# Kernel tuning notes

Hardware: AMD Instinct MI355X
Metric: run time of the kernel (lower is better)

Reference implementation:

```python
import jax, jax.numpy as jnp
import numpy as np

B, N, M, K = 4, 8192, 2048, 8
F1, F2 = 256, 256


def _knn_idx(p1t, p2t, k):
    # p1t [B,N,3], p2t [B,M,3] -> idx [B,N,k] of k nearest points in p2t for each p1t point
    d = (jnp.sum(p1t ** 2, -1)[:, :, None]
         + jnp.sum(p2t ** 2, -1)[:, None, :]
         - 2.0 * jnp.einsum('bnc,bmc->bnm', p1t, p2t))
    _, idx = jax.lax.top_k(-d, k)
    return idx


def _gather(feat, idx):
    # feat [B,C,M], idx [B,N,K] -> [B,C,N,K]  (grouping_operation)
    return jax.vmap(lambda f, i: f[:, i])(feat, idx)


def setup_inputs() -> dict:
    key = jax.random.key(0)
    ks = jax.random.split(key, 16)
    rn = lambda k, s: jax.random.normal(k, s, dtype=jnp.float32)
    ru = lambda k, s: jax.random.uniform(k, s, dtype=jnp.float32)
    return {
        'pos1': rn(ks[0], (B, 3, N)),
        'pos2': rn(ks[1], (B, 3, M)),
        'feature1': rn(ks[2], (B, F1, N)),
        'feature2': rn(ks[3], (B, F2, M)),
        'w1_0': rn(ks[4], (128, F2 + 3)) * 0.05, 's1_0': ru(ks[5], (128,)), 'b1_0': rn(ks[6], (128,)) * 0.05,
        'w1_1': rn(ks[7], (128, 128)) * 0.05, 's1_1': ru(ks[8], (128,)), 'b1_1': rn(ks[9], (128,)) * 0.05,
        'w1_2': rn(ks[10], (256, 128)) * 0.05, 's1_2': ru(ks[11], (256,)), 'b1_2': rn(ks[12], (256,)) * 0.05,
        'w2_0': rn(ks[13], (256, 256 + F1)) * 0.05, 's2_0': ru(ks[14], (256,)), 'b2_0': rn(ks[15], (256,)) * 0.05,
    }


def reference(pos1, pos2, feature1, feature2,
              w1_0, s1_0, b1_0, w1_1, s1_1, b1_1, w1_2, s1_2, b1_2,
              w2_0, s2_0, b2_0):
    # KNN grouping (knn=True branch): neighbors of each pos1 point among pos2 points
    idx = _knn_idx(pos1.transpose(0, 2, 1), pos2.transpose(0, 2, 1), K)  # [B,N,K]
    pos2_grouped = _gather(pos2, idx)                 # [B,3,N,K]
    pos_diff = pos2_grouped - pos1[:, :, :, None]     # [B,3,N,K]
    feat2_grouped = _gather(feature2, idx)            # [B,F2,N,K]
    feat = jnp.concatenate([feat2_grouped, pos_diff], axis=1)  # [B,F2+3,N,K]
    # mlp1: 1x1 Conv2d (no bias) + BN(eval, folded scale/bias) + ReLU
    for w, s, b in ((w1_0, s1_0, b1_0), (w1_1, s1_1, b1_1), (w1_2, s1_2, b1_2)):
        feat = jax.nn.relu(jnp.einsum('oc,bcnk->bonk', w, feat)
                           * s[None, :, None, None] + b[None, :, None, None])
    feat = jnp.max(feat, axis=-1)                     # [B,256,N]
    feat = jnp.concatenate([feat, feature1], axis=1)  # [B,256+F1,N]
    # mlp2: 1x1 Conv1d (no bias) + BN + ReLU
    for w, s, b in ((w2_0, s2_0, b2_0),):
        feat = jax.nn.relu(jnp.einsum('oc,bcn->bon', w, feat)
                           * s[None, :, None] + b[None, :, None])
    return feat
```

## Files before the change

### kernel.cpp

```cpp
#include <hip/hip_runtime.h>
#include <hip/hip_bf16.h>

#define B_ 4
#define N_ 8192
#define M_ 2048
#define K_ 8

typedef __bf16 bf16x8 __attribute__((ext_vector_type(8)));
typedef __bf16 bf16x4 __attribute__((ext_vector_type(4)));
typedef float  floatx4 __attribute__((ext_vector_type(4)));
typedef unsigned long long u64k;

__global__ __launch_bounds__(256) void preproc(
    const float* __restrict__ w10, const float* __restrict__ w11,
    const float* __restrict__ w12, const float* __restrict__ w20,
    const float* __restrict__ feature2,
    __bf16* __restrict__ w0p, __bf16* __restrict__ w11b,
    __bf16* __restrict__ w12b, __bf16* __restrict__ w20b,
    __bf16* __restrict__ f2t)
{
  __shared__ float tile[32][33];
  const int bid = blockIdx.x;
  if (bid < 2048) {
    const int C = 256, L = M_;
    const int b = bid >> 9;
    const int c0 = ((bid >> 6) & 7) * 32, l0 = (bid & 63) * 32;
    const int tx = threadIdx.x & 31, ty = threadIdx.x >> 5;
    const float* src = feature2 + (size_t)b * C * L;
    #pragma unroll
    for (int i = 0; i < 4; i++)
      tile[ty + 8 * i][tx] = src[(size_t)(c0 + ty + 8 * i) * L + l0 + tx];
    __syncthreads();
    __bf16* dst = f2t + (size_t)b * L * C;
    #pragma unroll
    for (int i = 0; i < 4; i++)
      dst[(size_t)(l0 + ty + 8 * i) * C + c0 + tx] = (__bf16)tile[tx][ty + 8 * i];
  } else {
    int t = (bid - 2048) * 256 + threadIdx.x;
    if (t < 36864) {
      int o = t / 288, c = t - o * 288;
      w0p[t] = (c < 259) ? (__bf16)w10[o * 259 + c] : (__bf16)0.0f;
    } else if (t < 53248) {
      int i = t - 36864; w11b[i] = (__bf16)w11[i];
    } else if (t < 86016) {
      int i = t - 53248; w12b[i] = (__bf16)w12[i];
    } else if (t < 217088) {
      int i = t - 86016; w20b[i] = (__bf16)w20[i];
    }
  }
}

__device__ __forceinline__ void ce(u64k& a, u64k& b) {
  u64k lo = a < b ? a : b;
  u64k hi = a < b ? b : a;
  a = lo; b = hi;
}

__global__ __launch_bounds__(256, 4) void knn_kernel(
    const float* __restrict__ pos1, const float* __restrict__ pos2,
    u64k* __restrict__ part)
{
  __shared__ floatx4 P[1024];
  __shared__ u64k md[64][33];
  const int b = blockIdx.y;
  const int half = blockIdx.z;
  const int n0 = blockIdx.x * 64;
  const int tid = threadIdx.x;
  const int cbase = half * 1024;

  const float* p2 = pos2 + b * 3 * M_;
  for (int i = tid; i < 1024; i += 256) {
    const int c = cbase + i;
    float x = p2[c], y = p2[M_ + c], z = p2[2 * M_ + c];
    floatx4 q;
    q[0] = x; q[1] = y; q[2] = z;
    q[3] = __fadd_rn(__fadd_rn(__fmul_rn(x, x), __fmul_rn(y, y)), __fmul_rn(z, z));
    P[i] = q;
  }
  __syncthreads();

  const int p = tid >> 2, t = tid & 3;
  const int n = n0 + p;
  const float* p1 = pos1 + b * 3 * N_;
  const float x1 = p1[n], y1 = p1[N_ + n], z1 = p1[2 * N_ + n];
  const float r1 = __fadd_rn(__fadd_rn(__fmul_rn(x1, x1), __fmul_rn(y1, y1)),
                             __fmul_rn(z1, z1));

  u64k bd[8];
  #pragma unroll
  for (int r = 0; r < 8; r++) bd[r] = ~0ULL;

  for (int bb = 0; bb < 32; ++bb) {
    floatx4 q[8];
    #pragma unroll
    for (int i = 0; i < 8; i++) q[i] = P[4 * (8 * bb + i) + t];

    u64k s[8];
    #pragma unroll
    for (int i = 0; i < 8; i++) {
      float dot = __fadd_rn(__fadd_rn(__fmul_rn(x1, q[i][0]), __fmul_rn(y1, q[i][1])),
                            __fmul_rn(z1, q[i][2]));
      float d = __fsub_rn(__fadd_rn(r1, q[i][3]), __fmul_rn(2.0f, dot));
      unsigned du = __float_as_uint(d);
      unsigned k32 = du ^ ((unsigned)((int)du >> 31) | 0x80000000u);
      s[i] = ((u64k)k32 << 11) | (unsigned)(cbase + 4 * (8 * bb + i) + t);
    }

    ce(s[0], s[1]); ce(s[2], s[3]); ce(s[4], s[5]); ce(s[6], s[7]);
    ce(s[0], s[2]); ce(s[1], s[3]); ce(s[4], s[6]); ce(s[5], s[7]);
    ce(s[1], s[2]); ce(s[5], s[6]);
    ce(s[0], s[4]); ce(s[1], s[5]); ce(s[2], s[6]); ce(s[3], s[7]);
    ce(s[2], s[4]); ce(s[3], s[5]);
    ce(s[1], s[2]); ce(s[3], s[4]); ce(s[5], s[6]);

    if (s[0] < bd[7]) {
      #pragma unroll
      for (int k = 0; k < 8; k++) { u64k x = s[7 - k]; bd[k] = bd[k] < x ? bd[k] : x; }
      ce(bd[0], bd[4]); ce(bd[1], bd[5]); ce(bd[2], bd[6]); ce(bd[3], bd[7]);
      ce(bd[0], bd[2]); ce(bd[1], bd[3]); ce(bd[4], bd[6]); ce(bd[5], bd[7]);
      ce(bd[0], bd[1]); ce(bd[2], bd[3]); ce(bd[4], bd[5]); ce(bd[6], bd[7]);
    }
  }

  #pragma unroll
  for (int r = 0; r < 8; r++) md[p][t * 8 + r] = bd[r];
  __syncthreads();

  if (tid < 64) {
    int h0 = 0, h1 = 0, h2 = 0, h3 = 0;
    u64k* o = part + ((size_t)((b * 2 + half) * N_ + n0 + tid)) * 8;
    #pragma unroll
    for (int r = 0; r < 8; r++) {
      u64k k0 = md[tid][h0], k1 = md[tid][8 + h1];
      u64k k2 = md[tid][16 + h2], k3 = md[tid][24 + h3];
      u64k m01 = k0 < k1 ? k0 : k1;
      u64k m23 = k2 < k3 ? k2 : k3;
      u64k m = m01 < m23 ? m01 : m23;
      h0 += (k0 == m); h1 += (k1 == m); h2 += (k2 == m); h3 += (k3 == m);
      o[r] = m;
    }
  }
}

template <int KSTEPS>
__device__ __forceinline__ void mfma_kloop_swz(
    const __bf16* X, const __bf16* W, int wstride, int c0, int lane,
    floatx4 (&acc)[4][2])
{
  const int lrow = lane & 15, quad = lane >> 4;
  const floatx4 fz = {0.f, 0.f, 0.f, 0.f};
  #pragma unroll
  for (int pt = 0; pt < 4; pt++) { acc[pt][0] = fz; acc[pt][1] = fz; }

  bf16x8 wf0 = *(const bf16x8*)(W + (size_t)(c0 + lrow) * wstride + quad * 8);
  bf16x8 wf1 = *(const bf16x8*)(W + (size_t)(c0 + 16 + lrow) * wstride + quad * 8);
  bf16x8 xf[4];
  #pragma unroll
  for (int pt = 0; pt < 4; pt++) {
    const int row = pt * 16 + lrow;
    xf[pt] = *(const bf16x8*)((const char*)X + row * 256
                              + ((quad * 16) ^ ((row & 7) << 4)));
  }

  #pragma unroll
  for (int ks = 0; ks < KSTEPS; ks++) {
    bf16x8 wn0, wn1, xn[4];
    if (ks + 1 < KSTEPS) {
      const int kn = (ks + 1) * 32 + quad * 8;
      wn0 = *(const bf16x8*)(W + (size_t)(c0 + lrow) * wstride + kn);
      wn1 = *(const bf16x8*)(W + (size_t)(c0 + 16 + lrow) * wstride + kn);
      #pragma unroll
      for (int pt = 0; pt < 4; pt++) {
        const int row = pt * 16 + lrow;
        xn[pt] = *(const bf16x8*)((const char*)X + row * 256
                                  + (((ks + 1) * 64 + quad * 16) ^ ((row & 7) << 4)));
      }
    }
    #pragma unroll
    for (int pt = 0; pt < 4; pt++) {
      acc[pt][0] = __builtin_amdgcn_mfma_f32_16x16x32_bf16(wf0, xf[pt], acc[pt][0], 0, 0, 0);
      acc[pt][1] = __builtin_amdgcn_mfma_f32_16x16x32_bf16(wf1, xf[pt], acc[pt][1], 0, 0, 0);
    }
    if (ks + 1 < KSTEPS) {
      wf0 = wn0; wf1 = wn1;
      #pragma unroll
      for (int pt = 0; pt < 4; pt++) xf[pt] = xn[pt];
    }
  }
}

__global__ __launch_bounds__(256, 3) void mlp1_kernel(
    const float* __restrict__ pos1, const float* __restrict__ pos2,
    const u64k* __restrict__ part, const __bf16* __restrict__ f2t,
    const __bf16* __restrict__ w0p, const float* __restrict__ s10, const float* __restrict__ b10,
    const __bf16* __restrict__ w11b, const float* __restrict__ s11, const float* __restrict__ b11,
    const __bf16* __restrict__ w12b, const float* __restrict__ s12, const float* __restrict__ b12,
    __bf16* __restrict__ maxed)
{
  __shared__ __align__(16) __bf16 Xs[64 * 256];
  __shared__ int mrow[64];
  __bf16* const Y1 = Xs;
  __bf16* const Y0 = Xs + 32 * 256;
  __bf16* const Mst = Xs + 32 * 256;

  const int b = blockIdx.y;
  const int n0 = blockIdx.x * 8;
  const int tid = threadIdx.x;
  const int wave = tid >> 6, lane = tid & 63;
  const int lrow = lane & 15, quad = lane >> 4;
  const int c0 = 32 * wave;

  if (tid < 8) {
    const u64k* a0 = part + ((size_t)((b * 2 + 0) * N_ + n0 + tid)) * 8;
    const u64k* a1 = part + ((size_t)((b * 2 + 1) * N_ + n0 + tid)) * 8;
    u64k av[8], cv[8];
    #pragma unroll
    for (int r = 0; r < 8; r++) { av[r] = a0[r]; cv[r] = a1[r]; }
    #pragma unroll
    for (int k = 0; k < 8; k++) { u64k x = cv[7 - k]; av[k] = av[k] < x ? av[k] : x; }
    ce(av[0], av[4]); ce(av[1], av[5]); ce(av[2], av[6]); ce(av[3], av[7]);
    ce(av[0], av[2]); ce(av[1], av[3]); ce(av[4], av[6]); ce(av[5], av[7]);
    ce(av[0], av[1]); ce(av[2], av[3]); ce(av[4], av[5]); ce(av[6], av[7]);
    #pragma unroll
    for (int r = 0; r < 8; r++) mrow[tid * 8 + r] = (int)(av[r] & 2047u);
  }
  __syncthreads();

  {
    const int r0 = wave * 16;
    const int hf = lane >> 5;
    const int ch = lane & 31;
    #pragma unroll
    for (int i = 0; i < 8; i++) {
      const int r = r0 + 2 * i + hf;
      const int m = mrow[r];
      const char* src = (const char*)f2t
          + (((size_t)(b * M_ + m)) << 9)
          + ((ch << 4) ^ ((r & 7) << 4));
      __builtin_amdgcn_global_load_lds(
          (const __attribute__((address_space(1))) unsigned int*)src,
          (__attribute__((address_space(3))) unsigned int*)(Xs + (r0 + 2 * i) * 256),
          16, 0, 0);
    }
  }

  bf16x8 xlast[4];
  #pragma unroll
  for (int pt = 0; pt < 4; pt++) { bf16x8 v = {}; xlast[pt] = v; }
  if (quad == 0) {
    #pragma unroll
    for (int pt = 0; pt < 4; pt++) {
      const int r = pt * 16 + lrow;
      const int m = mrow[r];
      const int n = n0 + (r >> 3);
      bf16x8 v = {};
      v[0] = (__bf16)(pos2[b * 3 * M_ + m]          - pos1[b * 3 * N_ + n]);
      v[1] = (__bf16)(pos2[b * 3 * M_ + M_ + m]     - pos1[b * 3 * N_ + N_ + n]);
      v[2] = (__bf16)(pos2[b * 3 * M_ + 2 * M_ + m] - pos1[b * 3 * N_ + 2 * N_ + n]);
      xlast[pt] = v;
    }
  }

  bf16x8 wf0 = *(const bf16x8*)(w0p + (size_t)(c0 + lrow) * 288 + quad * 8);
  bf16x8 wf1 = *(const bf16x8*)(w0p + (size_t)(c0 + 16 + lrow) * 288 + quad * 8);

  __syncthreads();

  floatx4 acc[4][2];
  {
    const floatx4 fz = {0.f, 0.f, 0.f, 0.f};
    #pragma unroll
    for (int pt = 0; pt < 4; pt++) { acc[pt][0] = fz; acc[pt][1] = fz; }

    const int swz = (lrow & 7) << 4;
    bf16x8 xf[4];
    #pragma unroll
    for (int pt = 0; pt < 4; pt++)
      xf[pt] = *(const bf16x8*)((const char*)Xs + (pt * 16 + lrow) * 512
                                + ((quad * 16) ^ swz));

    #pragma unroll
    for (int ks = 0; ks < 9; ks++) {
      bf16x8 wn0, wn1, xn[4];
      if (ks < 8) {
        const int kn = (ks + 1) * 32 + quad * 8;
        wn0 = *(const bf16x8*)(w0p + (size_t)(c0 + lrow) * 288 + kn);
        wn1 = *(const bf16x8*)(w0p + (size_t)(c0 + 16 + lrow) * 288 + kn);
        if (ks < 7) {
          const int kb = ((ks + 1) * 64 + quad * 16) ^ swz;
          #pragma unroll
          for (int pt = 0; pt < 4; pt++)
            xn[pt] = *(const bf16x8*)((const char*)Xs + (pt * 16 + lrow) * 512 + kb);
        } else {
          #pragma unroll
          for (int pt = 0; pt < 4; pt++) xn[pt] = xlast[pt];
        }
      }
      #pragma unroll
      for (int pt = 0; pt < 4; pt++) {
        acc[pt][0] = __builtin_amdgcn_mfma_f32_16x16x32_bf16(wf0, xf[pt], acc[pt][0], 0, 0, 0);
        acc[pt][1] = __builtin_amdgcn_mfma_f32_16x16x32_bf16(wf1, xf[pt], acc[pt][1], 0, 0, 0);
      }
      if (ks < 8) {
        wf0 = wn0; wf1 = wn1;
        #pragma unroll
        for (int pt = 0; pt < 4; pt++) xf[pt] = xn[pt];
      }
    }
  }

  __syncthreads();

  #pragma unroll
  for (int pt = 0; pt < 4; pt++) {
    #pragma unroll
    for (int wt = 0; wt < 2; wt++) {
      const int colg = c0 + wt * 16 + quad * 4;
      floatx4 s4 = *(const floatx4*)(s10 + colg);
      floatx4 b4 = *(const floatx4*)(b10 + colg);
      bf16x4 pk;
      #pragma unroll
      for (int r = 0; r < 4; r++) {
        float v = acc[pt][wt][r] * s4[r] + b4[r];
        pk[r] = (__bf16)(v > 0.f ? v : 0.f);
      }
      const int row = pt * 16 + lrow;
      const int cb = colg * 2;
      *(bf16x4*)((char*)Y0 + row * 256
                 + ((cb & ~15) ^ ((row & 7) << 4)) + (cb & 15)) = pk;
    }
  }
  __syncthreads();

  {
    floatx4 a1c[4][2];
    mfma_kloop_swz<4>(Y0, w11b, 128, c0, lane, a1c);
    #pragma unroll
    for (int pt = 0; pt < 4; pt++) {
      #pragma unroll
      for (int wt = 0; wt < 2; wt++) {
        const int colg = c0 + wt * 16 + quad * 4;
        floatx4 s4 = *(const floatx4*)(s11 + colg);
        floatx4 b4 = *(const floatx4*)(b11 + colg);
        bf16x4 pk;
        #pragma unroll
        for (int r = 0; r < 4; r++) {
          float v = a1c[pt][wt][r] * s4[r] + b4[r];
          pk[r] = (__bf16)(v > 0.f ? v : 0.f);
        }
        const int row = pt * 16 + lrow;
        const int cb = colg * 2;
        *(bf16x4*)((char*)Y1 + row * 256
                   + ((cb & ~15) ^ ((row & 7) << 4)) + (cb & 15)) = pk;
      }
    }
  }
  __syncthreads();

  #pragma unroll
  for (int p = 0; p < 2; p++) {
    floatx4 a2c[4][2];
    mfma_kloop_swz<4>(Y1, w12b, 128, 128 * p + c0, lane, a2c);
    #pragma unroll
    for (int pt = 0; pt < 4; pt++) {
      #pragma unroll
      for (int wt = 0; wt < 2; wt++) {
        const int colg = 128 * p + c0 + wt * 16 + quad * 4;
        floatx4 s4 = *(const floatx4*)(s12 + colg);
        floatx4 b4 = *(const floatx4*)(b12 + colg);
        floatx4 v;
        #pragma unroll
        for (int r = 0; r < 4; r++) {
          float t = a2c[pt][wt][r] * s4[r] + b4[r];
          v[r] = t > 0.f ? t : 0.f;
        }
        #pragma unroll
        for (int st = 1; st <= 4; st <<= 1) {
          #pragma unroll
          for (int r = 0; r < 4; r++)
            v[r] = fmaxf(v[r], __shfl_xor(v[r], st, 64));
        }
        if ((lrow & 7) == 0) {
          const int point = pt * 2 + (lrow >> 3);
          bf16x4 pk;
          #pragma unroll
          for (int r = 0; r < 4; r++) pk[r] = (__bf16)v[r];
          *(bf16x4*)(Mst + point * 264 + colg) = pk;
        }
      }
    }
  }
  __syncthreads();

  {
    const int point = tid >> 5, ch = tid & 31;
    bf16x8 v = *(const bf16x8*)(Mst + point * 264 + ch * 8);
    *(bf16x8*)(maxed + ((size_t)(b * N_ + n0 + point)) * 256 + ch * 8) = v;
  }
}

__global__ __launch_bounds__(256, 4) void mlp2_kernel(
    const __bf16* __restrict__ maxed, const float* __restrict__ feature1,
    const __bf16* __restrict__ w20b, const float* __restrict__ s20,
    const float* __restrict__ b20, float* __restrict__ out)
{
  const int rows0 = blockIdx.x * 32;
  const int b = rows0 >> 13;
  const int nbase = rows0 & (N_ - 1);
  const int tid = threadIdx.x;
  const int wave = tid >> 6, lane = tid & 63;
  const int lrow = lane & 15, quad = lane >> 4;
  const int c0 = 128 * blockIdx.y + 32 * wave;
  const floatx4 fz = {0.f, 0.f, 0.f, 0.f};

  floatx4 acc[2][2];
  acc[0][0] = fz; acc[0][1] = fz; acc[1][0] = fz; acc[1][1] = fz;

  auto afrag = [&](int ks, int mt) -> bf16x8 {
    const int k = ks * 32 + quad * 8;
    if (ks < 8) {
      return *(const bf16x8*)(maxed + (size_t)(rows0 + mt * 16 + lrow) * 256 + k);
    } else {
      const int c = k - 256;
      const float* p = feature1 + ((size_t)(b * 256 + c)) * N_
                       + (nbase + mt * 16 + lrow);
      bf16x8 v;
      #pragma unroll
      for (int j = 0; j < 8; j++) v[j] = (__bf16)p[(size_t)j * N_];
      return v;
    }
  };

  bf16x8 w0 = *(const bf16x8*)(w20b + (size_t)(c0 + lrow) * 512 + quad * 8);
  bf16x8 w1 = *(const bf16x8*)(w20b + (size_t)(c0 + 16 + lrow) * 512 + quad * 8);
  bf16x8 a0 = afrag(0, 0);
  bf16x8 a1 = afrag(0, 1);

  #pragma unroll
  for (int ks = 0; ks < 16; ks++) {
    bf16x8 wn0, wn1, an0, an1;
    if (ks < 15) {
      const int kn = (ks + 1) * 32 + quad * 8;
      wn0 = *(const bf16x8*)(w20b + (size_t)(c0 + lrow) * 512 + kn);
      wn1 = *(const bf16x8*)(w20b + (size_t)(c0 + 16 + lrow) * 512 + kn);
      an0 = afrag(ks + 1, 0);
      an1 = afrag(ks + 1, 1);
    }
    acc[0][0] = __builtin_amdgcn_mfma_f32_16x16x32_bf16(a0, w0, acc[0][0], 0, 0, 0);
    acc[0][1] = __builtin_amdgcn_mfma_f32_16x16x32_bf16(a0, w1, acc[0][1], 0, 0, 0);
    acc[1][0] = __builtin_amdgcn_mfma_f32_16x16x32_bf16(a1, w0, acc[1][0], 0, 0, 0);
    acc[1][1] = __builtin_amdgcn_mfma_f32_16x16x32_bf16(a1, w1, acc[1][1], 0, 0, 0);
    if (ks < 15) { w0 = wn0; w1 = wn1; a0 = an0; a1 = an1; }
  }

  #pragma unroll
  for (int ct = 0; ct < 2; ct++) {
    const int col = c0 + ct * 16 + lrow;
    const float s = s20[col];
    const float bb = b20[col];
    #pragma unroll
    for (int mt = 0; mt < 2; mt++) {
      floatx4 pk;
      #pragma unroll
      for (int r = 0; r < 4; r++) {
        float v = acc[mt][ct][r] * s + bb;
        pk[r] = v > 0.f ? v : 0.f;
      }
      const int n = nbase + mt * 16 + quad * 4;
      *(floatx4*)(out + ((size_t)(b * 256 + col)) * N_ + n) = pk;
    }
  }
}

extern "C" void kernel_launch(void* const* d_in, const int* in_sizes, int n_in,
                              void* d_out, int out_size, void* d_ws, size_t ws_size,
                              hipStream_t stream)
{
  const float* pos1     = (const float*)d_in[0];
  const float* pos2     = (const float*)d_in[1];
  const float* feature1 = (const float*)d_in[2];
  const float* feature2 = (const float*)d_in[3];
  const float* w1_0 = (const float*)d_in[4];
  const float* s1_0 = (const float*)d_in[5];
  const float* b1_0 = (const float*)d_in[6];
  const float* w1_1 = (const float*)d_in[7];
  const float* s1_1 = (const float*)d_in[8];
  const float* b1_1 = (const float*)d_in[9];
  const float* w1_2 = (const float*)d_in[10];
  const float* s1_2 = (const float*)d_in[11];
  const float* b1_2 = (const float*)d_in[12];
  const float* w2_0 = (const float*)d_in[13];
  const float* s2_0 = (const float*)d_in[14];
  const float* b2_0 = (const float*)d_in[15];

  char* ws = (char*)d_ws;
  __bf16* f2t   = (__bf16*)(ws + 1048576);
  u64k*   part  = (u64k*)(ws + 5242880);
  __bf16* maxed = (__bf16*)(ws + 22020096);
  __bf16* w0p   = (__bf16*)(ws + 38797312);
  __bf16* w11b  = (__bf16*)(ws + 38871040);
  __bf16* w12b  = (__bf16*)(ws + 38903808);
  __bf16* w20b  = (__bf16*)(ws + 38969344);

  preproc<<<dim3(2896), 256, 0, stream>>>(w1_0, w1_1, w1_2, w2_0, feature2,
                                          w0p, w11b, w12b, w20b, f2t);
  knn_kernel<<<dim3(N_ / 64, B_, 2), 256, 0, stream>>>(pos1, pos2, part);
  mlp1_kernel<<<dim3(N_ / 8, B_), 256, 0, stream>>>(
      pos1, pos2, part, f2t, w0p, s1_0, b1_0, w11b, s1_1, b1_1, w12b, s1_2, b1_2, maxed);
  mlp2_kernel<<<dim3(1024, 2), 256, 0, stream>>>(maxed, feature1, w20b, s2_0, b2_0,
                                                 (float*)d_out);
}
```

Baseline: 344.9 us.

## Fuse KNN into preprocessing kernel and emit final int indices

The KNN search moves into the preprocessing launch as the first 512 blocks. Each block now scans all 2048 candidates instead of splitting them across two halves, and writes final int32 indices rather than two partial u64 top-8 lists that mlp1 had to merge. mlp1 now reads the indices directly from global memory, drops its merge step and the shared index array, and raises its occupancy hint from 3 to 4. This removes one kernel launch and the partial-list traffic, but halves KNN parallelism (512 long blocks), enlarges the fused kernel's shared memory to about 49 KB, and adds register pressure from the higher occupancy target.

```diff
diff --git a/kernel.cpp b/kernel.cpp
--- a/kernel.cpp
+++ b/kernel.cpp
@@ -11,21 +11,109 @@
 typedef float  floatx4 __attribute__((ext_vector_type(4)));
 typedef unsigned long long u64k;
 
-__global__ __launch_bounds__(256) void preproc(
+__device__ __forceinline__ void ce(u64k& a, u64k& b) {
+  u64k lo = a < b ? a : b;
+  u64k hi = a < b ? b : a;
+  a = lo; b = hi;
+}
+
+__global__ __launch_bounds__(256) void pre_knn(
     const float* __restrict__ w10, const float* __restrict__ w11,
     const float* __restrict__ w12, const float* __restrict__ w20,
     const float* __restrict__ feature2,
+    const float* __restrict__ pos1, const float* __restrict__ pos2,
     __bf16* __restrict__ w0p, __bf16* __restrict__ w11b,
     __bf16* __restrict__ w12b, __bf16* __restrict__ w20b,
-    __bf16* __restrict__ f2t)
+    __bf16* __restrict__ f2t, int* __restrict__ idx_out)
 {
-  __shared__ float tile[32][33];
+  __shared__ __align__(16) char smem[49664];
   const int bid = blockIdx.x;
-  if (bid < 2048) {
+  const int tid = threadIdx.x;
+
+  if (bid < 512) {
+    floatx4* P = (floatx4*)smem;
+    u64k (*md)[33] = (u64k(*)[33])(smem + 32768);
+    const int b = bid >> 7;
+    const int n0 = (bid & 127) * 64;
+
+    const float* p2 = pos2 + b * 3 * M_;
+    for (int i = tid; i < M_; i += 256) {
+      float x = p2[i], y = p2[M_ + i], z = p2[2 * M_ + i];
+      floatx4 q;
+      q[0] = x; q[1] = y; q[2] = z;
+      q[3] = __fadd_rn(__fadd_rn(__fmul_rn(x, x), __fmul_rn(y, y)), __fmul_rn(z, z));
+      P[i] = q;
+    }
+    __syncthreads();
+
+    const int p = tid >> 2, t = tid & 3;
+    const int n = n0 + p;
+    const float* p1 = pos1 + b * 3 * N_;
+    const float x1 = p1[n], y1 = p1[N_ + n], z1 = p1[2 * N_ + n];
+    const float r1 = __fadd_rn(__fadd_rn(__fmul_rn(x1, x1), __fmul_rn(y1, y1)),
+                               __fmul_rn(z1, z1));
+
+    u64k bd[8];
+    #pragma unroll
+    for (int r = 0; r < 8; r++) bd[r] = ~0ULL;
+
+    for (int bb = 0; bb < 64; ++bb) {
+      floatx4 q[8];
+      #pragma unroll
+      for (int i = 0; i < 8; i++) q[i] = P[4 * (8 * bb + i) + t];
+
+      u64k s[8];
+      #pragma unroll
+      for (int i = 0; i < 8; i++) {
+        float dot = __fadd_rn(__fadd_rn(__fmul_rn(x1, q[i][0]), __fmul_rn(y1, q[i][1])),
+                              __fmul_rn(z1, q[i][2]));
+        float d = __fsub_rn(__fadd_rn(r1, q[i][3]), __fmul_rn(2.0f, dot));
+        unsigned du = __float_as_uint(d);
+        unsigned k32 = du ^ ((unsigned)((int)du >> 31) | 0x80000000u);
+        s[i] = ((u64k)k32 << 11) | (unsigned)(4 * (8 * bb + i) + t);
+      }
+
+      ce(s[0], s[1]); ce(s[2], s[3]); ce(s[4], s[5]); ce(s[6], s[7]);
+      ce(s[0], s[2]); ce(s[1], s[3]); ce(s[4], s[6]); ce(s[5], s[7]);
+      ce(s[1], s[2]); ce(s[5], s[6]);
+      ce(s[0], s[4]); ce(s[1], s[5]); ce(s[2], s[6]); ce(s[3], s[7]);
+      ce(s[2], s[4]); ce(s[3], s[5]);
+      ce(s[1], s[2]); ce(s[3], s[4]); ce(s[5], s[6]);
+
+      if (s[0] < bd[7]) {
+        #pragma unroll
+        for (int k = 0; k < 8; k++) { u64k x = s[7 - k]; bd[k] = bd[k] < x ? bd[k] : x; }
+        ce(bd[0], bd[4]); ce(bd[1], bd[5]); ce(bd[2], bd[6]); ce(bd[3], bd[7]);
+        ce(bd[0], bd[2]); ce(bd[1], bd[3]); ce(bd[4], bd[6]); ce(bd[5], bd[7]);
+        ce(bd[0], bd[1]); ce(bd[2], bd[3]); ce(bd[4], bd[5]); ce(bd[6], bd[7]);
+      }
+    }
+
+    #pragma unroll
+    for (int r = 0; r < 8; r++) md[p][t * 8 + r] = bd[r];
+    __syncthreads();
+
+    if (tid < 64) {
+      int h0 = 0, h1 = 0, h2 = 0, h3 = 0;
+      int* o = idx_out + ((size_t)(b * N_ + n0 + tid)) * 8;
+      #pragma unroll
+      for (int r = 0; r < 8; r++) {
+        u64k k0 = md[tid][h0], k1 = md[tid][8 + h1];
+        u64k k2 = md[tid][16 + h2], k3 = md[tid][24 + h3];
+        u64k m01 = k0 < k1 ? k0 : k1;
+        u64k m23 = k2 < k3 ? k2 : k3;
+        u64k m = m01 < m23 ? m01 : m23;
+        h0 += (k0 == m); h1 += (k1 == m); h2 += (k2 == m); h3 += (k3 == m);
+        o[r] = (int)(m & 2047u);
+      }
+    }
+  } else if (bid < 2560) {
+    float (*tile)[33] = (float(*)[33])smem;
+    const int tb = bid - 512;
     const int C = 256, L = M_;
-    const int b = bid >> 9;
-    const int c0 = ((bid >> 6) & 7) * 32, l0 = (bid & 63) * 32;
-    const int tx = threadIdx.x & 31, ty = threadIdx.x >> 5;
+    const int b = tb >> 9;
+    const int c0 = ((tb >> 6) & 7) * 32, l0 = (tb & 63) * 32;
+    const int tx = tid & 31, ty = tid >> 5;
     const float* src = feature2 + (size_t)b * C * L;
     #pragma unroll
     for (int i = 0; i < 4; i++)
@@ -36,7 +124,7 @@
     for (int i = 0; i < 4; i++)
       dst[(size_t)(l0 + ty + 8 * i) * C + c0 + tx] = (__bf16)tile[tx][ty + 8 * i];
   } else {
-    int t = (bid - 2048) * 256 + threadIdx.x;
+    int t = (bid - 2560) * 256 + tid;
     if (t < 36864) {
       int o = t / 288, c = t - o * 288;
       w0p[t] = (c < 259) ? (__bf16)w10[o * 259 + c] : (__bf16)0.0f;
@@ -50,98 +138,6 @@
   }
 }
 
-__device__ __forceinline__ void ce(u64k& a, u64k& b) {
-  u64k lo = a < b ? a : b;
-  u64k hi = a < b ? b : a;
-  a = lo; b = hi;
-}
-
-__global__ __launch_bounds__(256, 4) void knn_kernel(
-    const float* __restrict__ pos1, const float* __restrict__ pos2,
-    u64k* __restrict__ part)
-{
-  __shared__ floatx4 P[1024];
-  __shared__ u64k md[64][33];
-  const int b = blockIdx.y;
-  const int half = blockIdx.z;
-  const int n0 = blockIdx.x * 64;
-  const int tid = threadIdx.x;
-  const int cbase = half * 1024;
-
-  const float* p2 = pos2 + b * 3 * M_;
-  for (int i = tid; i < 1024; i += 256) {
-    const int c = cbase + i;
-    float x = p2[c], y = p2[M_ + c], z = p2[2 * M_ + c];
-    floatx4 q;
-    q[0] = x; q[1] = y; q[2] = z;
-    q[3] = __fadd_rn(__fadd_rn(__fmul_rn(x, x), __fmul_rn(y, y)), __fmul_rn(z, z));
-    P[i] = q;
-  }
-  __syncthreads();
-
-  const int p = tid >> 2, t = tid & 3;
-  const int n = n0 + p;
-  const float* p1 = pos1 + b * 3 * N_;
-  const float x1 = p1[n], y1 = p1[N_ + n], z1 = p1[2 * N_ + n];
-  const float r1 = __fadd_rn(__fadd_rn(__fmul_rn(x1, x1), __fmul_rn(y1, y1)),
-                             __fmul_rn(z1, z1));
-
-  u64k bd[8];
-  #pragma unroll
-  for (int r = 0; r < 8; r++) bd[r] = ~0ULL;
-
-  for (int bb = 0; bb < 32; ++bb) {
-    floatx4 q[8];
-    #pragma unroll
-    for (int i = 0; i < 8; i++) q[i] = P[4 * (8 * bb + i) + t];
-
-    u64k s[8];
-    #pragma unroll
-    for (int i = 0; i < 8; i++) {
-      float dot = __fadd_rn(__fadd_rn(__fmul_rn(x1, q[i][0]), __fmul_rn(y1, q[i][1])),
-                            __fmul_rn(z1, q[i][2]));
-      float d = __fsub_rn(__fadd_rn(r1, q[i][3]), __fmul_rn(2.0f, dot));
-      unsigned du = __float_as_uint(d);
-      unsigned k32 = du ^ ((unsigned)((int)du >> 31) | 0x80000000u);
-      s[i] = ((u64k)k32 << 11) | (unsigned)(cbase + 4 * (8 * bb + i) + t);
-    }
-
-    ce(s[0], s[1]); ce(s[2], s[3]); ce(s[4], s[5]); ce(s[6], s[7]);
-    ce(s[0], s[2]); ce(s[1], s[3]); ce(s[4], s[6]); ce(s[5], s[7]);
-    ce(s[1], s[2]); ce(s[5], s[6]);
-    ce(s[0], s[4]); ce(s[1], s[5]); ce(s[2], s[6]); ce(s[3], s[7]);
-    ce(s[2], s[4]); ce(s[3], s[5]);
-    ce(s[1], s[2]); ce(s[3], s[4]); ce(s[5], s[6]);
-
-    if (s[0] < bd[7]) {
-      #pragma unroll
-      for (int k = 0; k < 8; k++) { u64k x = s[7 - k]; bd[k] = bd[k] < x ? bd[k] : x; }
-      ce(bd[0], bd[4]); ce(bd[1], bd[5]); ce(bd[2], bd[6]); ce(bd[3], bd[7]);
-      ce(bd[0], bd[2]); ce(bd[1], bd[3]); ce(bd[4], bd[6]); ce(bd[5], bd[7]);
-      ce(bd[0], bd[1]); ce(bd[2], bd[3]); ce(bd[4], bd[5]); ce(bd[6], bd[7]);
-    }
-  }
-
-  #pragma unroll
-  for (int r = 0; r < 8; r++) md[p][t * 8 + r] = bd[r];
-  __syncthreads();
-
-  if (tid < 64) {
-    int h0 = 0, h1 = 0, h2 = 0, h3 = 0;
-    u64k* o = part + ((size_t)((b * 2 + half) * N_ + n0 + tid)) * 8;
-    #pragma unroll
-    for (int r = 0; r < 8; r++) {
-      u64k k0 = md[tid][h0], k1 = md[tid][8 + h1];
-      u64k k2 = md[tid][16 + h2], k3 = md[tid][24 + h3];
-      u64k m01 = k0 < k1 ? k0 : k1;
-      u64k m23 = k2 < k3 ? k2 : k3;
-      u64k m = m01 < m23 ? m01 : m23;
-      h0 += (k0 == m); h1 += (k1 == m); h2 += (k2 == m); h3 += (k3 == m);
-      o[r] = m;
-    }
-  }
-}
-
 template <int KSTEPS>
 __device__ __forceinline__ void mfma_kloop_swz(
     const __bf16* X, const __bf16* W, int wstride, int c0, int lane,
@@ -189,16 +185,15 @@
   }
 }
 
-__global__ __launch_bounds__(256, 3) void mlp1_kernel(
+__global__ __launch_bounds__(256, 4) void mlp1_kernel(
     const float* __restrict__ pos1, const float* __restrict__ pos2,
-    const u64k* __restrict__ part, const __bf16* __restrict__ f2t,
+    const int* __restrict__ idx, const __bf16* __restrict__ f2t,
     const __bf16* __restrict__ w0p, const float* __restrict__ s10, const float* __restrict__ b10,
     const __bf16* __restrict__ w11b, const float* __restrict__ s11, const float* __restrict__ b11,
     const __bf16* __restrict__ w12b, const float* __restrict__ s12, const float* __restrict__ b12,
     __bf16* __restrict__ maxed)
 {
   __shared__ __align__(16) __bf16 Xs[64 * 256];
-  __shared__ int mrow[64];
   __bf16* const Y1 = Xs;
   __bf16* const Y0 = Xs + 32 * 256;
   __bf16* const Mst = Xs + 32 * 256;
@@ -209,33 +204,21 @@
   const int wave = tid >> 6, lane = tid & 63;
   const int lrow = lane & 15, quad = lane >> 4;
   const int c0 = 32 * wave;
-
-  if (tid < 8) {
-    const u64k* a0 = part + ((size_t)((b * 2 + 0) * N_ + n0 + tid)) * 8;
-    const u64k* a1 = part + ((size_t)((b * 2 + 1) * N_ + n0 + tid)) * 8;
-    u64k av[8], cv[8];
-    #pragma unroll
-    for (int r = 0; r < 8; r++) { av[r] = a0[r]; cv[r] = a1[r]; }
-    #pragma unroll
-    for (int k = 0; k < 8; k++) { u64k x = cv[7 - k]; av[k] = av[k] < x ? av[k] : x; }
-    ce(av[0], av[4]); ce(av[1], av[5]); ce(av[2], av[6]); ce(av[3], av[7]);
-    ce(av[0], av[2]); ce(av[1], av[3]); ce(av[4], av[6]); ce(av[5], av[7]);
-    ce(av[0], av[1]); ce(av[2], av[3]); ce(av[4], av[5]); ce(av[6], av[7]);
-    #pragma unroll
-    for (int r = 0; r < 8; r++) mrow[tid * 8 + r] = (int)(av[r] & 2047u);
-  }
-  __syncthreads();
+  const int idxbase = (b * N_ + n0) * K_;
 
   {
     const int r0 = wave * 16;
     const int hf = lane >> 5;
     const int ch = lane & 31;
+    int mr[8];
+    #pragma unroll
+    for (int i = 0; i < 8; i++)
+      mr[i] = idx[idxbase + r0 + 2 * i + hf];
     #pragma unroll
     for (int i = 0; i < 8; i++) {
       const int r = r0 + 2 * i + hf;
-      const int m = mrow[r];
       const char* src = (const char*)f2t
-          + (((size_t)(b * M_ + m)) << 9)
+          + (((size_t)(b * M_ + mr[i])) << 9)
           + ((ch << 4) ^ ((r & 7) << 4));
       __builtin_amdgcn_global_load_lds(
           (const __attribute__((address_space(1))) unsigned int*)src,
@@ -251,7 +234,7 @@
     #pragma unroll
     for (int pt = 0; pt < 4; pt++) {
       const int r = pt * 16 + lrow;
-      const int m = mrow[r];
+      const int m = idx[idxbase + r];
       const int n = n0 + (r >> 3);
       bf16x8 v = {};
       v[0] = (__bf16)(pos2[b * 3 * M_ + m]          - pos1[b * 3 * N_ + n]);
@@ -494,19 +477,19 @@
   const float* b2_0 = (const float*)d_in[15];
 
   char* ws = (char*)d_ws;
+  int*    idx   = (int*)(ws);
   __bf16* f2t   = (__bf16*)(ws + 1048576);
-  u64k*   part  = (u64k*)(ws + 5242880);
   __bf16* maxed = (__bf16*)(ws + 22020096);
   __bf16* w0p   = (__bf16*)(ws + 38797312);
   __bf16* w11b  = (__bf16*)(ws + 38871040);
   __bf16* w12b  = (__bf16*)(ws + 38903808);
   __bf16* w20b  = (__bf16*)(ws + 38969344);
 
-  preproc<<<dim3(2896), 256, 0, stream>>>(w1_0, w1_1, w1_2, w2_0, feature2,
-                                          w0p, w11b, w12b, w20b, f2t);
-  knn_kernel<<<dim3(N_ / 64, B_, 2), 256, 0, stream>>>(pos1, pos2, part);
+  pre_knn<<<dim3(3408), 256, 0, stream>>>(
+      w1_0, w1_1, w1_2, w2_0, feature2, pos1, pos2,
+      w0p, w11b, w12b, w20b, f2t, idx);
   mlp1_kernel<<<dim3(N_ / 8, B_), 256, 0, stream>>>(
-      pos1, pos2, part, f2t, w0p, s1_0, b1_0, w11b, s1_1, b1_1, w12b, s1_2, b1_2, maxed);
+      pos1, pos2, idx, f2t, w0p, s1_0, b1_0, w11b, s1_1, b1_1, w12b, s1_2, b1_2, maxed);
   mlp2_kernel<<<dim3(1024, 2), 256, 0, stream>>>(maxed, feature1, w20b, s2_0, b2_0,
                                                  (float*)d_out);
 }
```

Result: no change. 349.2 us (+1.2%).
